# Kernel tuning notes

Measured on AMD Instinct MI355X. Metric: run time of the kernel, lower is better.

Reference implementation:

```python
import jax, jax.numpy as jnp
import numpy as np

T = 2048          # tokens (single-sequence prefill)
HIDDEN = 2048
H = 32            # attention heads
NOPE, ROPE, VD = 128, 64, 128
QLORA, KVLORA = 1536, 512
IDX_H, IDX_D, TOPK = 32, 128, 512
EPS = 1e-6
BASE = 10000.0
SCALE = float((NOPE + ROPE) ** -0.5)
IDX_SCALE = float(IDX_D ** -0.5)
FP8_MAX = 448.0
NEG = -1e30


def _rope_tables(positions, dim):
    inv = 1.0 / (BASE ** (jnp.arange(0, dim, 2, dtype=jnp.float32) / dim))
    ang = positions.astype(jnp.float32)[:, None] * inv[None, :]
    return jnp.cos(ang), jnp.sin(ang)  # [T, dim//2]


def _rot_interleaved(x, cos, sin):
    # GPT-J style (is_neox_style=False): pairs (x[2i], x[2i+1]). x: [T, nH, d]
    Tn, nH, d = x.shape
    xr = x.reshape(Tn, nH, d // 2, 2)
    x1, x2 = xr[..., 0], xr[..., 1]
    c, s = cos[:, None, :], sin[:, None, :]
    o1 = x1 * c - x2 * s
    o2 = x2 * c + x1 * s
    return jnp.stack([o1, o2], axis=-1).reshape(Tn, nH, d)


def _rot_neox(x, cos, sin):
    # half-split rotation (is_neox_style=True). x: [T, nH, d]
    d = x.shape[-1] // 2
    x1, x2 = x[..., :d], x[..., d:]
    c, s = cos[:, None, :], sin[:, None, :]
    return jnp.concatenate([x1 * c - x2 * s, x2 * c + x1 * s], axis=-1)


def _rms_norm(x, w):
    return x * jax.lax.rsqrt(jnp.mean(x * x, axis=-1, keepdims=True) + EPS) * w


def _layer_norm(x, g, b):
    m = jnp.mean(x, axis=-1, keepdims=True)
    v = jnp.mean((x - m) ** 2, axis=-1, keepdims=True)
    return (x - m) * jax.lax.rsqrt(v + 1e-6) * g + b


def _quant_fp8_ue8m0(x):
    # per-128-group fp8 quant; IDX_D == group size so one group per row
    amax = jnp.maximum(jnp.max(jnp.abs(x), axis=-1, keepdims=True), 1e-10)
    scale = jnp.exp2(jnp.ceil(jnp.log2(amax / FP8_MAX)))  # ue8m0: pow-2 scale
    q = (x / scale).astype(jnp.float8_e4m3fn).astype(jnp.float32)
    return q, scale


def setup_inputs() -> dict:
    ks = jax.random.split(jax.random.key(0), 12)
    def w(i, shape):
        return jax.random.normal(ks[i], shape, jnp.float32) * 0.02
    return {
        "positions": jnp.arange(T, dtype=jnp.int32),
        "hidden_states": jax.random.normal(ks[0], (T, HIDDEN), jnp.float32),
        "q_c": jax.random.normal(ks[1], (T, QLORA), jnp.float32),
        "kv_lora": jax.random.normal(ks[2], (T, KVLORA + ROPE), jnp.float32),
        "W_qb": w(3, (QLORA, H * (NOPE + ROPE))),
        "W_kvb": w(4, (KVLORA, H * (NOPE + VD))),
        "W_o": w(5, (H * VD, HIDDEN)),
        "kv_a_ln_w": jnp.ones((KVLORA,), jnp.float32),
        "W_iq": w(6, (QLORA, IDX_H * IDX_D)),
        "W_ik": w(7, (HIDDEN, IDX_D)),
        "ik_gamma": jnp.ones((IDX_D,), jnp.float32),
        "ik_beta": jnp.zeros((IDX_D,), jnp.float32),
        "W_iw": w(8, (HIDDEN, IDX_H)),
    }


def _indexer_topk(positions, hidden_states, q_c, W_iq, W_ik, ik_gamma, ik_beta, W_iw):
    # lightning indexer: per-query top-K token selection
    q = (q_c @ W_iq).reshape(T, IDX_H, IDX_D)
    q_pe, q_nope = q[..., :ROPE], q[..., ROPE:]
    k = _layer_norm(hidden_states @ W_ik, ik_gamma, ik_beta)  # [T, IDX_D]
    k_pe, k_nope = k[:, :ROPE], k[:, ROPE:]
    cos, sin = _rope_tables(positions, ROPE)
    q_pe = _rot_neox(q_pe, cos, sin)
    k_pe = _rot_neox(k_pe[:, None, :], cos, sin)[:, 0]
    q = jnp.concatenate([q_pe, q_nope], axis=-1)        # [T, IDX_H, IDX_D]
    k = jnp.concatenate([k_pe, k_nope], axis=-1)        # [T, IDX_D]
    q_fp8, q_scale = _quant_fp8_ue8m0(q)                # scale [T, IDX_H, 1]
    k_fp8, k_scale = _quant_fp8_ue8m0(k)                # scale [T, 1]
    weights = (hidden_states @ W_iw) * q_scale[..., 0] * IDX_SCALE * (IDX_H ** -0.5)
    logits = jnp.einsum("thd,sd->hts", q_fp8, k_fp8) * k_scale[:, 0][None, None, :]
    score = jnp.einsum("th,hts->ts", weights, jax.nn.relu(logits))  # [T, S]
    causal = positions[:, None] >= positions[None, :]
    score = jnp.where(causal, score, NEG)
    topk_idx = jax.lax.top_k(score, TOPK)[1]            # [T, TOPK]
    return topk_idx, causal


def reference(positions, hidden_states, q_c, kv_lora, W_qb, W_kvb, W_o,
              kv_a_ln_w, W_iq, W_ik, ik_gamma, ik_beta, W_iw):
    # 1. Q B-projection + split
    q = (q_c @ W_qb).reshape(T, H, NOPE + ROPE)
    q_nope, q_pe = q[..., :NOPE], q[..., NOPE:]
    # 2. KV layernorm + RoPE (interleaved / non-neox)
    kv_c, k_pe = kv_lora[:, :KVLORA], kv_lora[:, KVLORA:]
    kv_c = _rms_norm(kv_c, kv_a_ln_w)
    cos, sin = _rope_tables(positions, ROPE)
    q_pe = _rot_interleaved(q_pe, cos, sin)             # [T, H, ROPE]
    k_pe = _rot_interleaved(k_pe[:, None, :], cos, sin)[:, 0]  # [T, ROPE]
    # 3. sparse indexer
    topk_idx, causal = _indexer_topk(positions, hidden_states, q_c,
                                     W_iq, W_ik, ik_gamma, ik_beta, W_iw)
    allowed = jnp.zeros((T, T), bool).at[jnp.arange(T)[:, None], topk_idx].set(True)
    allowed = allowed & causal
    # 5. W_UK_T absorption
    w_kvb = W_kvb.reshape(KVLORA, H, NOPE + VD)
    W_UK, W_UV = w_kvb[..., :NOPE], w_kvb[..., NOPE:]   # [r,H,n], [r,H,v]
    q_lat = jnp.einsum("thn,rhn->thr", q_nope, W_UK)    # [T, H, r]
    # 6. sparse MQA attention in latent space
    scores = (jnp.einsum("thr,sr->hts", q_lat, kv_c)
              + jnp.einsum("thp,sp->hts", q_pe, k_pe)) * SCALE
    scores = jnp.where(allowed[None], scores, NEG)
    probs = jax.nn.softmax(scores, axis=-1)
    o_lat = jnp.einsum("hts,sr->thr", probs, kv_c)      # [T, H, r]
    # 7. W_UV up-projection, 8. o_proj
    v = jnp.einsum("thr,rhv->thv", o_lat, W_UV)         # [T, H, VD]
    return v.reshape(T, H * VD) @ W_o                   # [T, HIDDEN]
```

## Files before the change

kernel.cpp:

```cpp
#include <hip/hip_runtime.h>
#include <hip/hip_bf16.h>

#define T_N    2048
#define H_N    32
#define NOPE_N 128
#define ROPE_N 64
#define VD_N   128
#define QLORA_N 1536
#define KVLORA_N 512
#define IDX_H_N 32
#define IDX_D_N 128
#define TOPK_N 512
#define HID_N  2048

typedef __attribute__((ext_vector_type(8))) short bf16x8;
typedef __attribute__((ext_vector_type(4))) float f32x4;
typedef unsigned short ushortT;
typedef unsigned char uchar;

#define SCALE_F 0.07216878364870323f

static __device__ __forceinline__ ushortT f2bf(float x) {
    __hip_bfloat16 b = __float2bfloat16(x);
    return *(ushortT*)&b;
}
static __device__ __forceinline__ float bf2f(ushortT u) {
    __hip_bfloat16 b = *(__hip_bfloat16*)&u;
    return __bfloat162float(b);
}

static __device__ __forceinline__ float q_e4m3(float x) {
    float ax = fabsf(x);
    unsigned b = __float_as_uint(ax);
    int e = (int)(b >> 23) - 126;
    int ue = (e - 4 > -9) ? (e - 4) : -9;
    float ulp = __int_as_float((ue + 127) << 23);
    float q = rintf(ax / ulp) * ulp;
    return copysignf(q, x);
}

static __device__ __forceinline__ uchar enc_e4m3(float q) {
    unsigned b = __float_as_uint(q);
    unsigned s = (b >> 31) << 7;
    float ax = fabsf(q);
    if (ax == 0.f) return (uchar)s;
    int e = (int)((b >> 23) & 255) - 127;
    if (e >= -6) {
        unsigned m = (b >> 20) & 7;
        return (uchar)(s | ((unsigned)(e + 7) << 3) | m);
    }
    unsigned M = (unsigned)rintf(ax * 512.f);
    return (uchar)(s | M);
}

__global__ void k_rope_tables(const int* __restrict__ pos, float* __restrict__ cosT,
                              float* __restrict__ sinT) {
    int t = blockIdx.x, i = threadIdx.x;
    double inv = 1.0 / pow(10000.0, (double)i / 32.0);
    double ang = (double)pos[t] * inv;
    cosT[t * 32 + i] = (float)cos(ang);
    sinT[t * 32 + i] = (float)sin(ang);
}

template <bool BT>
__global__ __launch_bounds__(256) void gemm128(
    const float* __restrict__ A, const float* __restrict__ B, float* __restrict__ C,
    int M, int N, int K, int lda, int ldb, int ldc,
    long batchOffA, long batchOffB, long batchOffC) {
    const float* Ab = A + (size_t)batchOffA * blockIdx.z;
    const float* Bb = B + (size_t)batchOffB * blockIdx.z;
    int bm = blockIdx.y * 128, bn = blockIdx.x * 128;
    int tid = threadIdx.x;
    __shared__ float As[8][128];
    __shared__ float Bs[8][128];
    float acc[8][8];
#pragma unroll
    for (int i = 0; i < 8; ++i)
#pragma unroll
        for (int j = 0; j < 8; ++j) acc[i][j] = 0.f;
    int tx = tid & 15, ty = tid >> 4;
    int ar = tid >> 1, ak = (tid & 1) * 4;
    for (int k0 = 0; k0 < K; k0 += 8) {
        float4 av = *(const float4*)(Ab + (size_t)(bm + ar) * lda + k0 + ak);
        As[ak + 0][ar] = av.x; As[ak + 1][ar] = av.y;
        As[ak + 2][ar] = av.z; As[ak + 3][ar] = av.w;
        if (BT) {
            int n = tid >> 1, kk = (tid & 1) * 4;
            float4 bv = *(const float4*)(Bb + (size_t)(bn + n) * ldb + k0 + kk);
            Bs[kk + 0][n] = bv.x; Bs[kk + 1][n] = bv.y;
            Bs[kk + 2][n] = bv.z; Bs[kk + 3][n] = bv.w;
        } else {
            int kk = tid >> 5, n = (tid & 31) * 4;
            float4 bv = *(const float4*)(Bb + (size_t)(k0 + kk) * ldb + bn + n);
            Bs[kk][n + 0] = bv.x; Bs[kk][n + 1] = bv.y;
            Bs[kk][n + 2] = bv.z; Bs[kk][n + 3] = bv.w;
        }
        __syncthreads();
#pragma unroll
        for (int kk = 0; kk < 8; ++kk) {
            float4 a0 = *(const float4*)(&As[kk][ty * 8]);
            float4 a1 = *(const float4*)(&As[kk][ty * 8 + 4]);
            float4 b0 = *(const float4*)(&Bs[kk][tx * 8]);
            float4 b1 = *(const float4*)(&Bs[kk][tx * 8 + 4]);
            float a[8] = {a0.x, a0.y, a0.z, a0.w, a1.x, a1.y, a1.z, a1.w};
            float b[8] = {b0.x, b0.y, b0.z, b0.w, b1.x, b1.y, b1.z, b1.w};
#pragma unroll
            for (int i = 0; i < 8; ++i)
#pragma unroll
                for (int j = 0; j < 8; ++j) acc[i][j] = fmaf(a[i], b[j], acc[i][j]);
        }
        __syncthreads();
    }
    size_t cbase = (size_t)batchOffC * blockIdx.z;
#pragma unroll
    for (int i = 0; i < 8; ++i) {
        size_t r = bm + ty * 8 + i;
#pragma unroll
        for (int j = 0; j < 8; ++j) {
            size_t c = bn + tx * 8 + j;
            C[cbase + r * (size_t)ldc + c] = acc[i][j];
        }
    }
}

template <bool CB16>
__global__ __launch_bounds__(256) void bgemm(
    const ushortT* __restrict__ A, const ushortT* __restrict__ B, void* __restrict__ Cv,
    int K, int lda, int ldb, int ldc,
    long boffA, long boffB, long boffC, float scaleC) {
    const ushortT* Ab = A + (size_t)boffA * blockIdx.z;
    const ushortT* Bb = B + (size_t)boffB * blockIdx.z;
    int bm = blockIdx.y * 128, bn = blockIdx.x * 128;
    int tid = threadIdx.x, lane = tid & 63, w = tid >> 6;
    int wr = w >> 1, wc = w & 1;
    int lr = lane & 15, lk = lane >> 4;

    __shared__ __align__(16) ushortT sbuf[16384];
    ushortT* As = sbuf;
    ushortT* Bs = sbuf + 8192;

    f32x4 acc[4][4];
#pragma unroll
    for (int i = 0; i < 4; ++i)
#pragma unroll
        for (int j = 0; j < 4; ++j) acc[i][j] = (f32x4){0.f, 0.f, 0.f, 0.f};

    for (int kt = 0; kt < K; kt += 64) {
        __syncthreads();
#pragma unroll
        for (int q = 0; q < 4; ++q) {
            int ch = tid + q * 256;
            int row = ch >> 3, e8 = ch & 7;
            int byteoff = (row * 128 + e8 * 16) ^ ((row & 7) << 4);
            uint4 va = *(const uint4*)(Ab + (size_t)(bm + row) * lda + kt + e8 * 8);
            *(uint4*)((char*)As + byteoff) = va;
            uint4 vb = *(const uint4*)(Bb + (size_t)(bn + row) * ldb + kt + e8 * 8);
            *(uint4*)((char*)Bs + byteoff) = vb;
        }
        __syncthreads();
#pragma unroll
        for (int kk = 0; kk < 2; ++kk) {
            bf16x8 af[4], bfr[4];
#pragma unroll
            for (int i = 0; i < 4; ++i) {
                int arow = wr * 64 + i * 16 + lr;
                af[i] = *(const bf16x8*)((const char*)As +
                         ((arow * 128 + kk * 64 + lk * 16) ^ ((arow & 7) << 4)));
                int brow = wc * 64 + i * 16 + lr;
                bfr[i] = *(const bf16x8*)((const char*)Bs +
                         ((brow * 128 + kk * 64 + lk * 16) ^ ((brow & 7) << 4)));
            }
#pragma unroll
            for (int i = 0; i < 4; ++i)
#pragma unroll
                for (int j = 0; j < 4; ++j)
                    acc[i][j] = __builtin_amdgcn_mfma_f32_16x16x32_bf16(af[i], bfr[j], acc[i][j], 0, 0, 0);
        }
    }
    size_t cbase = (size_t)boffC * blockIdx.z;
    if (CB16) {
        __syncthreads();
#pragma unroll
        for (int mi = 0; mi < 4; ++mi)
#pragma unroll
            for (int ni = 0; ni < 4; ++ni)
#pragma unroll
                for (int r = 0; r < 4; ++r) {
                    int row = wr * 64 + mi * 16 + lk * 4 + r;
                    int col = wc * 64 + ni * 16 + lr;
                    int off = (row * 256 + col * 2) ^ ((row & 7) << 4);
                    *(ushortT*)((char*)sbuf + off) = f2bf(acc[mi][ni][r] * scaleC);
                }
        __syncthreads();
        ushortT* outp = (ushortT*)Cv;
#pragma unroll
        for (int i = 0; i < 8; ++i) {
            int idx = i * 256 + tid;
            int row = idx >> 4, seg = idx & 15;
            uint4 v = *(const uint4*)((const char*)sbuf +
                       ((row * 256 + seg * 16) ^ ((row & 7) << 4)));
            *(uint4*)(outp + cbase + (size_t)(bm + row) * ldc + bn + seg * 8) = v;
        }
    } else {
#pragma unroll
        for (int mi = 0; mi < 4; ++mi)
#pragma unroll
            for (int ni = 0; ni < 4; ++ni) {
                int col = bn + wc * 64 + ni * 16 + lr;
#pragma unroll
                for (int r = 0; r < 4; ++r) {
                    int row = bm + wr * 64 + mi * 16 + lk * 4 + r;
                    ((float*)Cv)[cbase + (size_t)row * ldc + col] = acc[mi][ni][r];
                }
            }
    }
}

__global__ __launch_bounds__(256) void k_cast4(const float* __restrict__ src,
                                               ushortT* __restrict__ dst, int n4) {
    int i = blockIdx.x * 256 + threadIdx.x;
    if (i < n4) {
        float4 v = ((const float4*)src)[i];
        ushortT o[4] = {f2bf(v.x), f2bf(v.y), f2bf(v.z), f2bf(v.w)};
        *(uint2*)(dst + (size_t)i * 4) = *(uint2*)o;
    }
}

__global__ __launch_bounds__(256) void k_tcast(const float* __restrict__ src,
                                               ushortT* __restrict__ dst,
                                               long sa, long soff, long sz,
                                               long da, long dz) {
    __shared__ float tile[32][33];
    int a0 = blockIdx.x * 32, b0 = blockIdx.y * 32;
    int tx = threadIdx.x & 31, ty = threadIdx.x >> 5;
    const float* s = src + (size_t)sz * blockIdx.z + soff;
#pragma unroll
    for (int i = ty; i < 32; i += 8)
        tile[i][tx] = s[(size_t)(a0 + i) * sa + (b0 + tx)];
    __syncthreads();
    ushortT* d = dst + (size_t)dz * blockIdx.z;
#pragma unroll
    for (int i = ty; i < 32; i += 8)
        d[(size_t)(b0 + i) * da + a0 + tx] = f2bf(tile[tx][i]);
}

__global__ __launch_bounds__(256) void k_wuk_cast(const float* __restrict__ wkvb,
                                                  ushortT* __restrict__ wuk) {
    int i = blockIdx.x * 256 + threadIdx.x;
    int n = i & 127, r = (i >> 7) & 511, h = i >> 16;
    wuk[i] = f2bf(wkvb[(size_t)r * 8192 + h * 256 + n]);
}

__global__ __launch_bounds__(256) void k_kv_post2(const float* __restrict__ kv,
                                                  const float* __restrict__ lnw,
                                                  const float* __restrict__ cosT,
                                                  const float* __restrict__ sinT,
                                                  ushortT* __restrict__ kcat) {
    int t = blockIdx.x, tid = threadIdx.x;
    const float* row = kv + (size_t)t * 576;
    float v0 = row[tid], v1 = row[tid + 256];
    float s = v0 * v0 + v1 * v1;
    for (int o = 32; o > 0; o >>= 1) s += __shfl_down(s, o);
    __shared__ float sm[4];
    if ((tid & 63) == 0) sm[tid >> 6] = s;
    __syncthreads();
    float tot = sm[0] + sm[1] + sm[2] + sm[3];
    float inv = 1.f / sqrtf(tot / 512.f + 1e-6f);
    ushortT* out = kcat + (size_t)t * 576;
    out[tid] = f2bf(v0 * inv * lnw[tid]);
    out[tid + 256] = f2bf(v1 * inv * lnw[tid + 256]);
    if (tid < 32) {
        float c = cosT[t * 32 + tid], sn = sinT[t * 32 + tid];
        float x1 = row[512 + 2 * tid], x2 = row[512 + 2 * tid + 1];
        out[512 + 2 * tid] = f2bf(x1 * c - x2 * sn);
        out[512 + 2 * tid + 1] = f2bf(x2 * c + x1 * sn);
    }
}

__global__ __launch_bounds__(256) void k_rope_q2(const ushortT* __restrict__ qfull,
                                                 const float* __restrict__ cosT,
                                                 const float* __restrict__ sinT,
                                                 ushortT* __restrict__ qcat) {
    int b = blockIdx.x * 8 + (threadIdx.x >> 5);
    int i = threadIdx.x & 31;
    int t = b >> 5, h = b & 31;
    const ushortT* p = qfull + (size_t)b * 192 + 128;
    float c = cosT[t * 32 + i], s = sinT[t * 32 + i];
    float x1 = bf2f(p[2 * i]), x2 = bf2f(p[2 * i + 1]);
    ushortT* q = qcat + (size_t)t * 18432 + h * 576 + 512;
    q[2 * i] = f2bf((x1 * c - x2 * s) * SCALE_F);
    q[2 * i + 1] = f2bf((x2 * c + x1 * s) * SCALE_F);
}

__global__ __launch_bounds__(128) void k_ki_post16(const float* __restrict__ kp,
                                                   const float* __restrict__ g,
                                                   const float* __restrict__ be,
                                                   const float* __restrict__ cosT,
                                                   const float* __restrict__ sinT,
                                                   uchar* __restrict__ ki8,
                                                   float* __restrict__ kscale) {
    int t = blockIdx.x, i = threadIdx.x;
    float x = 0.f;
#pragma unroll
    for (int z = 0; z < 16; ++z) x += kp[(size_t)z * 262144 + (size_t)t * 128 + i];
    float s = x;
    for (int o = 32; o > 0; o >>= 1) s += __shfl_down(s, o);
    __shared__ float sm[2];
    if ((i & 63) == 0) sm[i >> 6] = s;
    __syncthreads();
    float mean = (sm[0] + sm[1]) / 128.f;
    float d = x - mean;
    float s2 = d * d;
    for (int o = 32; o > 0; o >>= 1) s2 += __shfl_down(s2, o);
    __shared__ float sv[2];
    if ((i & 63) == 0) sv[i >> 6] = s2;
    __syncthreads();
    float var = (sv[0] + sv[1]) / 128.f;
    float nrm = d * (1.f / sqrtf(var + 1e-6f)) * g[i] + be[i];
    __shared__ float buf[128];
    buf[i] = nrm;
    __syncthreads();
    float out;
    if (i < 32)      out = buf[i] * cosT[t * 32 + i] - buf[i + 32] * sinT[t * 32 + i];
    else if (i < 64) out = buf[i] * cosT[t * 32 + i - 32] + buf[i - 32] * sinT[t * 32 + i - 32];
    else             out = nrm;
    float a = fabsf(out);
    for (int o = 32; o > 0; o >>= 1) a = fmaxf(a, __shfl_down(a, o));
    __shared__ float am[2];
    if ((i & 63) == 0) am[i >> 6] = a;
    __syncthreads();
    float amax = fmaxf(fmaxf(am[0], am[1]), 1e-10f);
    float scale = __int_as_float((((int)ceilf(log2f(amax / 448.f))) + 127) << 23);
    ki8[(size_t)t * 128 + i] = enc_e4m3(q_e4m3(out / scale));
    if (i == 0) kscale[t] = scale;
}

__global__ __launch_bounds__(128) void k_qi_post_bf(const ushortT* __restrict__ qi_bf,
                                                    const float* __restrict__ cosT,
                                                    const float* __restrict__ sinT,
                                                    uchar* __restrict__ qi8,
                                                    float* __restrict__ qscale) {
    int b = blockIdx.x;
    int t = b >> 5;
    int i = threadIdx.x;
    float x = bf2f(qi_bf[(size_t)b * 128 + i]);
    __shared__ float buf[128];
    buf[i] = x;
    __syncthreads();
    float out;
    if (i < 32)      out = buf[i] * cosT[t * 32 + i] - buf[i + 32] * sinT[t * 32 + i];
    else if (i < 64) out = buf[i] * cosT[t * 32 + i - 32] + buf[i - 32] * sinT[t * 32 + i - 32];
    else             out = x;
    float a = fabsf(out);
    for (int o = 32; o > 0; o >>= 1) a = fmaxf(a, __shfl_down(a, o));
    __shared__ float am[2];
    if ((i & 63) == 0) am[i >> 6] = a;
    __syncthreads();
    float amax = fmaxf(fmaxf(am[0], am[1]), 1e-10f);
    float scale = __int_as_float((((int)ceilf(log2f(amax / 448.f))) + 127) << 23);
    qi8[(size_t)b * 128 + i] = enc_e4m3(q_e4m3(out / scale));
    if (i == 0) qscale[b] = scale;
}

__global__ __launch_bounds__(256) void k_wiw(const float* __restrict__ hs,
                                             const float* __restrict__ W_iw,
                                             const float* __restrict__ qscale,
                                             float* __restrict__ wts) {
    int t = blockIdx.x, tid = threadIdx.x;
    __shared__ float hr[2048];
    for (int i = tid; i < 2048; i += 256) hr[i] = hs[(size_t)t * 2048 + i];
    __syncthreads();
    int h = tid & 31, p = tid >> 5;
    float s = 0;
    for (int k = p * 256; k < p * 256 + 256; ++k) s = fmaf(hr[k], W_iw[(size_t)k * 32 + h], s);
    __shared__ float part[8][32];
    part[p][h] = s;
    __syncthreads();
    if (tid < 32) {
        float tot = 0;
#pragma unroll
        for (int pp = 0; pp < 8; ++pp) tot += part[pp][tid];
        const float a = (float)0.08838834764831845;
        const float b = (float)0.1767766952966369;
        wts[t * 32 + tid] = tot * qscale[t * 32 + tid] * a * b;
    }
}

__global__ __launch_bounds__(256) void k_score8(const uchar* __restrict__ qi8,
                                                const uchar* __restrict__ ki8,
                                                const float* __restrict__ kscale,
                                                const float* __restrict__ wts,
                                                float* __restrict__ score) {
    int b = blockIdx.x;
    int ti = (int)((sqrtf(8.f * b + 1.f) - 1.f) * 0.5f);
    while ((ti + 1) * (ti + 2) / 2 <= b) ++ti;
    while (ti * (ti + 1) / 2 > b) --ti;
    int si = b - ti * (ti + 1) / 2;
    int t0 = ti * 32, s0 = si * 32;
    int tid = threadIdx.x, lane = tid & 63, w = tid >> 6;
    int qt = w >> 1, qs = w & 1;
    int col = lane & 15, g = lane >> 4;

    __shared__ __align__(16) uchar k8s[4096];
    __shared__ __align__(16) uchar q8s[32768];
    __shared__ float wts_s[32][33];

    {
        int row = tid >> 3, inner = tid & 7;
        uint4 v = *(const uint4*)(ki8 + (size_t)(s0 + row) * 128 + inner * 16);
        *(uint4*)(k8s + ((row * 128 + inner * 16) ^ ((row & 7) << 4))) = v;
    }
    for (int c = tid; c < 1024; c += 256) {
        int tl = c >> 5, h = c & 31;
        wts_s[tl][h] = wts[(size_t)(t0 + tl) * 32 + h];
    }

    float ksc = kscale[s0 + qs * 16 + col];
    int arow = qt * 16 + col;
    int brow = qs * 16 + col;
    float sacc[4] = {0.f, 0.f, 0.f, 0.f};

    for (int h0 = 0; h0 < 32; h0 += 8) {
        __syncthreads();
        for (int c = tid; c < 2048; c += 256) {
            int hh = c >> 8, row = (c >> 3) & 31, inner = c & 7;
            uint4 v = *(const uint4*)(qi8 + ((size_t)(t0 + row) * 32 + h0 + hh) * 128 + inner * 16);
            *(uint4*)(q8s + hh * 4096 + ((row * 128 + inner * 16) ^ ((row & 7) << 4))) = v;
        }
        __syncthreads();
#pragma unroll
        for (int hh = 0; hh < 8; ++hh) {
            f32x4 c4 = (f32x4){0.f, 0.f, 0.f, 0.f};
#pragma unroll
            for (int kk = 0; kk < 4; ++kk) {
                long long a = *(const long long*)(q8s + hh * 4096 +
                              ((arow * 128 + kk * 32 + g * 8) ^ ((arow & 7) << 4)));
                long long bb = *(const long long*)(k8s +
                              ((brow * 128 + kk * 32 + g * 8) ^ ((brow & 7) << 4)));
                c4 = __builtin_amdgcn_mfma_f32_16x16x32_fp8_fp8(a, bb, c4, 0, 0, 0);
            }
            int h = h0 + hh;
#pragma unroll
            for (int r = 0; r < 4; ++r)
                sacc[r] = fmaf(fmaxf(c4[r] * ksc, 0.f), wts_s[qt * 16 + g * 4 + r][h], sacc[r]);
        }
    }
    int t = t0 + qt * 16 + g * 4;
    int s = s0 + qs * 16 + col;
#pragma unroll
    for (int r = 0; r < 4; ++r)
        if (s <= t + r) score[(size_t)(t + r) * T_N + s] = sacc[r];
}

__global__ __launch_bounds__(256) void k_topk(const float* __restrict__ score,
                                              int* __restrict__ tki, int* __restrict__ tkc) {
    int t = blockIdx.x;
    int n = t + 1;
    int tid = threadIdx.x;
    if (n <= TOPK_N) {
        for (int i = tid; i < n; i += 256) tki[(size_t)t * TOPK_N + i] = i;
        if (tid == 0) tkc[t] = n;
        return;
    }
    __shared__ unsigned keys[2048];
    const float* row = score + (size_t)t * T_N;
    for (int i = tid; i < n; i += 256) {
        float f = row[i] + 0.f;
        unsigned u = __float_as_uint(f);
        u = (u & 0x80000000u) ? ~u : (u | 0x80000000u);
        keys[i] = u;
    }
    __shared__ int hist[256];
    __shared__ unsigned sh_prefix;
    __shared__ int sh_need;
    if (tid == 0) { sh_prefix = 0u; sh_need = TOPK_N; }
    __syncthreads();
    unsigned maskHi = 0;
    for (int level = 3; level >= 0; --level) {
        hist[tid] = 0;
        __syncthreads();
        unsigned prefix = sh_prefix;
        int shift = level * 8;
        for (int i = tid; i < n; i += 256) {
            unsigned kk = keys[i];
            if ((kk & maskHi) == prefix) atomicAdd(&hist[(kk >> shift) & 255], 1);
        }
        __syncthreads();
        if (tid == 0) {
            int need = sh_need, cum = 0, bsel = 255;
            for (int bb = 255; bb >= 0; --bb) {
                if (cum + hist[bb] >= need) { bsel = bb; break; }
                cum += hist[bb];
            }
            sh_need = need - cum;
            sh_prefix = prefix | ((unsigned)bsel << shift);
        }
        __syncthreads();
        maskHi |= (0xFFu << shift);
    }
    unsigned thr = sh_prefix;
    int needEq = sh_need;
    int base = tid * 8;
    int eqcnt = 0;
#pragma unroll
    for (int j = 0; j < 8; ++j) {
        int i = base + j;
        if (i < n && keys[i] == thr) eqcnt++;
    }
    __shared__ int scn[256];
    scn[tid] = eqcnt;
    __syncthreads();
    for (int off = 1; off < 256; off <<= 1) {
        int add = (tid >= off) ? scn[tid - off] : 0;
        __syncthreads();
        scn[tid] += add;
        __syncthreads();
    }
    int eq_excl = scn[tid] - eqcnt;
    int acnt = 0;
    {
        int eqr = eq_excl;
#pragma unroll
        for (int j = 0; j < 8; ++j) {
            int i = base + j;
            if (i < n) {
                unsigned kk = keys[i];
                bool a = (kk > thr) || (kk == thr && eqr < needEq);
                if (kk == thr) eqr++;
                if (a) acnt++;
            }
        }
    }
    __syncthreads();
    scn[tid] = acnt;
    __syncthreads();
    for (int off = 1; off < 256; off <<= 1) {
        int add = (tid >= off) ? scn[tid - off] : 0;
        __syncthreads();
        scn[tid] += add;
        __syncthreads();
    }
    int pos = scn[tid] - acnt;
    {
        int eqr = eq_excl;
#pragma unroll
        for (int j = 0; j < 8; ++j) {
            int i = base + j;
            if (i < n) {
                unsigned kk = keys[i];
                bool a = (kk > thr) || (kk == thr && eqr < needEq);
                if (kk == thr) eqr++;
                if (a) tki[(size_t)t * TOPK_N + (pos++)] = i;
            }
        }
    }
    if (tid == 0) tkc[t] = TOPK_N;
}

__global__ __launch_bounds__(256, 2) void k_attn_mfma(const ushortT* __restrict__ qcat,
                                                      const ushortT* __restrict__ kcat,
                                                      const int* __restrict__ tki,
                                                      const int* __restrict__ tkc,
                                                      ushortT* __restrict__ olat) {
    int t = blockIdx.x;
    int tid = threadIdx.x;
    int lane = tid & 63;
    int w = tid >> 6;
    int S = tkc[t];
    int nchunk = (S + 31) >> 5;

    __shared__ int idx_s[512];
    __shared__ __align__(16) ushortT kbK[18 * 1024];
    __shared__ __align__(16) ushortT kbV[512 * 32];
    __shared__ __align__(16) ushortT psc[32 * 32];
    __shared__ float red[64];

    idx_s[tid] = (tid < S) ? tki[(size_t)t * TOPK_N + tid] : 0;
    idx_s[tid + 256] = (tid + 256 < S) ? tki[(size_t)t * TOPK_N + tid + 256] : 0;

    int lr = lane & 15, lk = lane >> 4;
    int mt = w >> 1, nt = w & 1;

    bf16x8 qf[18];
    {
        const ushortT* qrow = qcat + (size_t)t * 18432 + (size_t)(mt * 16 + lr) * 576 + lk * 8;
#pragma unroll
        for (int kk = 0; kk < 18; ++kk) qf[kk] = *(const bf16x8*)(qrow + kk * 32);
    }
    __syncthreads();

    int skey = (w << 3) | (lane >> 3);
    int part = lane & 7;

    f32x4 oa[2][8];
#pragma unroll
    for (int i = 0; i < 2; ++i)
#pragma unroll
        for (int j = 0; j < 8; ++j) oa[i][j] = (f32x4){0.f, 0.f, 0.f, 0.f};
    float sm_[4] = {0.f, 0.f, 0.f, 0.f};

    uint4 sv[9];
    {
        bool ok = skey < S;
        const ushortT* g = kcat + (size_t)idx_s[skey] * 576 + part * 8;
#pragma unroll
        for (int i = 0; i < 9; ++i) {
            uint4 v = {0, 0, 0, 0};
            if (ok) v = *(const uint4*)(g + i * 64);
            sv[i] = v;
        }
    }

    for (int p = 0; p < nchunk; ++p) {
#pragma unroll
        for (int i = 0; i < 9; ++i) {
            int dg = part + i * 8;
            int off = ((skey * 64 + (dg & 3) * 16) ^ ((skey & 7) << 4)) + (dg >> 2) * 2048;
            *(uint4*)((char*)kbK + off) = sv[i];
        }
#pragma unroll
        for (int i = 0; i < 8; ++i) {
            int dg = part + i * 8;
            int inner = ((((skey >> 3) + (dg & 3)) & 3) << 4) | ((skey & 7) << 1);
            const ushortT* pv = (const ushortT*)&sv[i];
#pragma unroll
            for (int j = 0; j < 8; ++j) {
                int off = ((dg * 8 + j) * 64 + inner) ^ (j << 4);
                *(ushortT*)((char*)kbV + off) = pv[j];
            }
        }
        __syncthreads();
        if (p + 1 < nchunk) {
            int gk = (p + 1) * 32 + skey;
            bool ok = gk < S;
            const ushortT* g = kcat + (size_t)idx_s[gk] * 576 + part * 8;
#pragma unroll
            for (int i = 0; i < 9; ++i) {
                uint4 v = {0, 0, 0, 0};
                if (ok) v = *(const uint4*)(g + i * 64);
                sv[i] = v;
            }
        }
        f32x4 acc = (f32x4){0.f, 0.f, 0.f, 0.f};
        int brow = nt * 16 + lr;
#pragma unroll
        for (int kk = 0; kk < 18; ++kk) {
            bf16x8 b = *(const bf16x8*)((const char*)kbK + kk * 2048 +
                        ((brow * 64 + lk * 16) ^ ((brow & 7) << 4)));
            acc = __builtin_amdgcn_mfma_f32_16x16x32_bf16(qf[kk], b, acc, 0, 0, 0);
        }
        int key_g = p * 32 + nt * 16 + lr;
        int hb = mt * 16 + lk * 4;
#pragma unroll
        for (int r = 0; r < 4; ++r) {
            float e = (key_g < S) ? expf(acc[r]) : 0.f;
            sm_[r] += e;
            int head = hb + r;
            int off = (head * 64 + (nt * 16 + lr) * 2) ^ ((head & 7) << 4);
            *(ushortT*)((char*)psc + off) = f2bf(e);
        }
        __syncthreads();
#pragma unroll
        for (int m2 = 0; m2 < 2; ++m2) {
            int arow = m2 * 16 + lr;
            bf16x8 a = *(const bf16x8*)((const char*)psc +
                        ((arow * 64 + lk * 16) ^ ((arow & 7) << 4)));
#pragma unroll
            for (int n2 = 0; n2 < 8; ++n2) {
                int dim = w * 128 + n2 * 16 + lr;
                int grp = (lk + ((dim >> 3) & 3)) & 3;
                bf16x8 b = *(const bf16x8*)((const char*)kbV +
                            ((dim * 64 + (grp << 4)) ^ ((dim & 7) << 4)));
                oa[m2][n2] = __builtin_amdgcn_mfma_f32_16x16x32_bf16(a, b, oa[m2][n2], 0, 0, 0);
            }
        }
        __syncthreads();
    }
#pragma unroll
    for (int off = 1; off < 16; off <<= 1)
#pragma unroll
        for (int r = 0; r < 4; ++r) sm_[r] += __shfl_xor(sm_[r], off);
    if (lr == 0) {
#pragma unroll
        for (int r = 0; r < 4; ++r) red[(mt * 16 + lk * 4 + r) * 2 + nt] = sm_[r];
    }
    __syncthreads();
#pragma unroll
    for (int m2 = 0; m2 < 2; ++m2)
#pragma unroll
        for (int r = 0; r < 4; ++r) {
            int head = m2 * 16 + lk * 4 + r;
            float dvv = 1.f / (red[head * 2] + red[head * 2 + 1]);
#pragma unroll
            for (int n2 = 0; n2 < 8; ++n2) {
                int dim = w * 128 + n2 * 16 + lr;
                int off = (head * 1024 + dim * 2) ^ ((head & 7) << 4);
                *(ushortT*)((char*)kbK + off) = f2bf(oa[m2][n2][r] * dvv);
            }
        }
    __syncthreads();
    ushortT* orow = olat + (size_t)t * 18432;
#pragma unroll
    for (int i = 0; i < 8; ++i) {
        int idx = i * 256 + tid;
        int head = idx >> 6, seg = idx & 63;
        uint4 v = *(const uint4*)((const char*)kbK +
                   ((head * 1024 + seg * 16) ^ ((head & 7) << 4)));
        *(uint4*)(orow + head * 512 + seg * 8) = v;
    }
}

extern "C" void kernel_launch(void* const* d_in, const int* in_sizes, int n_in,
                              void* d_out, int out_size, void* d_ws, size_t ws_size,
                              hipStream_t stream) {
    (void)in_sizes; (void)n_in; (void)out_size; (void)ws_size;
    const int*   positions = (const int*)d_in[0];
    const float* hs        = (const float*)d_in[1];
    const float* q_c       = (const float*)d_in[2];
    const float* kv_lora   = (const float*)d_in[3];
    const float* W_qb      = (const float*)d_in[4];
    const float* W_kvb     = (const float*)d_in[5];
    const float* W_o       = (const float*)d_in[6];
    const float* kv_ln     = (const float*)d_in[7];
    const float* W_iq      = (const float*)d_in[8];
    const float* W_ik      = (const float*)d_in[9];
    const float* gamma     = (const float*)d_in[10];
    const float* beta      = (const float*)d_in[11];
    const float* W_iw      = (const float*)d_in[12];

    float* ws = (float*)d_ws;
    float*   cosT   = ws;
    float*   sinT   = ws + 65536;
    int*     tki    = (int*)(ws + 131072);
    int*     tkc    = (int*)(ws + 1179648);
    ushortT* kcat   = (ushortT*)(ws + 1181696);
    float*   kscale = ws + 1771520;
    float*   qscale = ws + 1773568;
    float*   wts    = ws + 1839104;
    uchar*   qi8    = (uchar*)(ws + 1904640);
    uchar*   ki8    = (uchar*)(ws + 4001792);
    ushortT* qc_bf  = (ushortT*)(ws + 4067328);
    ushortT* wiq_t  = (ushortT*)(ws + 5640192);
    float*   kip    = ws + 8785920;
    ushortT* qi_bf  = (ushortT*)(ws + 12980224);
    ushortT* wqb_t  = (ushortT*)(ws + 5640192);
    ushortT* wuk_t  = (ushortT*)(ws + 10358784);
    ushortT* wuv_t  = (ushortT*)(ws + 11407360);
    ushortT* wo_t   = (ushortT*)(ws + 12980224);
    float*   score  = ws + 20844544;
    ushortT* vbuf   = (ushortT*)(ws + 20844544);
    ushortT* qfull_bf = (ushortT*)(ws + 25038848);
    ushortT* qcat   = (ushortT*)(ws + 31330304);

    k_rope_tables<<<T_N, 32, 0, stream>>>(positions, cosT, sinT);
    k_cast4<<<3072, 256, 0, stream>>>(q_c, qc_bf, T_N * QLORA_N / 4);
    k_tcast<<<dim3(48, 128, 1), 256, 0, stream>>>(W_iq, wiq_t, 4096, 0, 0, 1536, 0);
    gemm128<false><<<dim3(1, 16, 16), 256, 0, stream>>>(
        hs, W_ik, kip, T_N, 128, 128, HID_N, 128, 128, 128, 16384, 262144);
    k_ki_post16<<<T_N, 128, 0, stream>>>(kip, gamma, beta, cosT, sinT, ki8, kscale);
    bgemm<true><<<dim3(32, 16, 1), 256, 0, stream>>>(
        qc_bf, wiq_t, qi_bf, QLORA_N, QLORA_N, QLORA_N, 4096, 0, 0, 0, 1.f);
    k_qi_post_bf<<<T_N * IDX_H_N, 128, 0, stream>>>(qi_bf, cosT, sinT, qi8, qscale);
    k_wiw<<<T_N, 256, 0, stream>>>(hs, W_iw, qscale, wts);
    k_score8<<<2080, 256, 0, stream>>>(qi8, ki8, kscale, wts, score);
    k_topk<<<T_N, 256, 0, stream>>>(score, tki, tkc);
    k_kv_post2<<<T_N, 256, 0, stream>>>(kv_lora, kv_ln, cosT, sinT, kcat);
    k_tcast<<<dim3(48, 192, 1), 256, 0, stream>>>(W_qb, wqb_t, 6144, 0, 0, 1536, 0);
    k_wuk_cast<<<8192, 256, 0, stream>>>(W_kvb, wuk_t);
    k_tcast<<<dim3(16, 4, 32), 256, 0, stream>>>(W_kvb, wuv_t, 8192, 128, 256, 512, 65536);
    k_tcast<<<dim3(128, 64, 1), 256, 0, stream>>>(W_o, wo_t, 2048, 0, 0, 4096, 0);
    bgemm<true><<<dim3(48, 16, 1), 256, 0, stream>>>(
        qc_bf, wqb_t, qfull_bf, QLORA_N, QLORA_N, QLORA_N, 6144, 0, 0, 0, 1.f);
    k_rope_q2<<<T_N * H_N / 8, 256, 0, stream>>>(qfull_bf, cosT, sinT, qcat);
    bgemm<true><<<dim3(4, 16, 32), 256, 0, stream>>>(
        qfull_bf, wuk_t, qcat, NOPE_N, 6144, 128, 18432, 192, 65536, 576, SCALE_F);
    k_attn_mfma<<<T_N, 256, 0, stream>>>(qcat, kcat, tki, tkc, qcat);
    bgemm<true><<<dim3(1, 16, 32), 256, 0, stream>>>(
        qcat, wuv_t, vbuf, KVLORA_N, 18432, 512, 4096, 512, 65536, 128, 1.f);
    bgemm<false><<<dim3(16, 16, 1), 256, 0, stream>>>(
        vbuf, wo_t, (float*)d_out, H_N * VD_N, 4096, 4096, HID_N, 0, 0, 0, 1.f);
}
```

Baseline: 665.6 us.

## Double-buffer bgemm tiles via direct global-to-LDS loads and reswizzle V smem

The bf16 batched GEMM now loads tiles with global_load_lds straight into LDS, using a K step of 32 and two ping-pong buffers. The next tile's load is issued before computing the current one, so one barrier per iteration replaces the previous load-then-compute with two barriers. Separately, the sparse-attention kernel's V tile layout in shared memory gets an extra XOR term on writes and reads to reduce bank conflicts. Risks are the smaller K step per iteration, and correctness depends on the load and swizzle mappings lining up.

```diff
diff --git a/kernel.cpp b/kernel.cpp
--- a/kernel.cpp
+++ b/kernel.cpp
@@ -28,6 +28,10 @@
     __hip_bfloat16 b = *(__hip_bfloat16*)&u;
     return __bfloat162float(b);
 }
+
+#define GLL16(g, l) __builtin_amdgcn_global_load_lds( \
+    (const __attribute__((address_space(1))) unsigned int*)(g), \
+    (__attribute__((address_space(3))) unsigned int*)(l), 16, 0, 0)
 
 static __device__ __forceinline__ float q_e4m3(float x) {
     float ax = fabsf(x);
@@ -136,8 +140,19 @@
     int lr = lane & 15, lk = lane >> 4;
 
     __shared__ __align__(16) ushortT sbuf[16384];
-    ushortT* As = sbuf;
-    ushortT* Bs = sbuf + 8192;
+
+    const ushortT* gA[2];
+    const ushortT* gB[2];
+    unsigned ubase[2];
+#pragma unroll
+    for (int c = 0; c < 2; ++c) {
+        int p = w * 2048 + c * 1024 + (lane << 4);
+        int l = p ^ (((p >> 6) & 3) << 4);
+        int row = l >> 6, e8 = (l & 63) >> 4;
+        gA[c] = Ab + (size_t)(bm + row) * lda + e8 * 8;
+        gB[c] = Bb + (size_t)(bn + row) * ldb + e8 * 8;
+        ubase[c] = (unsigned)(w * 1024 + c * 512);
+    }
 
     f32x4 acc[4][4];
 #pragma unroll
@@ -145,37 +160,42 @@
 #pragma unroll
         for (int j = 0; j < 4; ++j) acc[i][j] = (f32x4){0.f, 0.f, 0.f, 0.f};
 
-    for (int kt = 0; kt < K; kt += 64) {
-        __syncthreads();
-#pragma unroll
-        for (int q = 0; q < 4; ++q) {
-            int ch = tid + q * 256;
-            int row = ch >> 3, e8 = ch & 7;
-            int byteoff = (row * 128 + e8 * 16) ^ ((row & 7) << 4);
-            uint4 va = *(const uint4*)(Ab + (size_t)(bm + row) * lda + kt + e8 * 8);
-            *(uint4*)((char*)As + byteoff) = va;
-            uint4 vb = *(const uint4*)(Bb + (size_t)(bn + row) * ldb + kt + e8 * 8);
-            *(uint4*)((char*)Bs + byteoff) = vb;
-        }
-        __syncthreads();
-#pragma unroll
-        for (int kk = 0; kk < 2; ++kk) {
-            bf16x8 af[4], bfr[4];
-#pragma unroll
-            for (int i = 0; i < 4; ++i) {
-                int arow = wr * 64 + i * 16 + lr;
-                af[i] = *(const bf16x8*)((const char*)As +
-                         ((arow * 128 + kk * 64 + lk * 16) ^ ((arow & 7) << 4)));
-                int brow = wc * 64 + i * 16 + lr;
-                bfr[i] = *(const bf16x8*)((const char*)Bs +
-                         ((brow * 128 + kk * 64 + lk * 16) ^ ((brow & 7) << 4)));
-            }
-#pragma unroll
-            for (int i = 0; i < 4; ++i)
-#pragma unroll
-                for (int j = 0; j < 4; ++j)
-                    acc[i][j] = __builtin_amdgcn_mfma_f32_16x16x32_bf16(af[i], bfr[j], acc[i][j], 0, 0, 0);
-        }
+    int nk = K >> 5;
+    int cur = 0;
+#pragma unroll
+    for (int c = 0; c < 2; ++c) {
+        GLL16(gA[c], &sbuf[ubase[c]]);
+        GLL16(gB[c], &sbuf[8192 + ubase[c]]);
+    }
+    for (int kt = 0; kt < nk; ++kt) {
+        __syncthreads();
+        if (kt + 1 < nk) {
+            int ko = (kt + 1) << 5;
+            int nb = (cur ^ 1) * 4096;
+#pragma unroll
+            for (int c = 0; c < 2; ++c) {
+                GLL16(gA[c] + ko, &sbuf[nb + ubase[c]]);
+                GLL16(gB[c] + ko, &sbuf[8192 + nb + ubase[c]]);
+            }
+        }
+        int abase = cur * 8192;
+        int bbase = 16384 + cur * 8192;
+        bf16x8 af[4], bfr[4];
+#pragma unroll
+        for (int i = 0; i < 4; ++i) {
+            int arow = wr * 64 + i * 16 + lr;
+            af[i] = *(const bf16x8*)((const char*)sbuf + abase +
+                     ((arow * 64 + lk * 16) ^ ((arow & 3) << 4)));
+            int brow = wc * 64 + i * 16 + lr;
+            bfr[i] = *(const bf16x8*)((const char*)sbuf + bbase +
+                     ((brow * 64 + lk * 16) ^ ((brow & 3) << 4)));
+        }
+#pragma unroll
+        for (int i = 0; i < 4; ++i)
+#pragma unroll
+            for (int j = 0; j < 4; ++j)
+                acc[i][j] = __builtin_amdgcn_mfma_f32_16x16x32_bf16(af[i], bfr[j], acc[i][j], 0, 0, 0);
+        cur ^= 1;
     }
     size_t cbase = (size_t)boffC * blockIdx.z;
     if (CB16) {
@@ -625,7 +645,7 @@
             const ushortT* pv = (const ushortT*)&sv[i];
 #pragma unroll
             for (int j = 0; j < 8; ++j) {
-                int off = ((dg * 8 + j) * 64 + inner) ^ (j << 4);
+                int off = ((dg * 8 + j) * 64 + inner) ^ (j << 4) ^ ((part & 4) << 4);
                 *(ushortT*)((char*)kbV + off) = pv[j];
             }
         }
@@ -670,7 +690,7 @@
                 int dim = w * 128 + n2 * 16 + lr;
                 int grp = (lk + ((dim >> 3) & 3)) & 3;
                 bf16x8 b = *(const bf16x8*)((const char*)kbV +
-                            ((dim * 64 + (grp << 4)) ^ ((dim & 7) << 4)));
+                            ((dim * 64 + (grp << 4)) ^ ((dim & 7) << 4) ^ (((dim >> 3) & 4) << 4)));
                 oa[m2][n2] = __builtin_amdgcn_mfma_f32_16x16x32_bf16(a, b, oa[m2][n2], 0, 0, 0);
             }
         }
```

Measured after the change: 762.3 us. 14.5% more time.
